# Optimization experiments

Measured on AMD Instinct MI355X. Metric: run time of the kernel, lower is better.

## Reference

```python
import jax, jax.numpy as jnp
import numpy as np

H = 768   # hidden_size
E = 9     # num_entity_types
R = 10    # num_relation_types
B, S, N = 8, 4096, 64
P = N * (N - 1) // 2  # 2016 ordered pairs i<j


def setup_inputs() -> dict:
    key = jax.random.key(0)
    ks = jax.random.split(key, 10)
    sd = 0.02
    return {
        "sequence_output": jax.random.normal(ks[0], (B, S, H), jnp.float32),
        "attention_mask": jnp.ones((B, S), jnp.int32),
        "entity_spans": jnp.sort(jax.random.randint(ks[1], (B, N, 2), 0, S), axis=-1),
        # entity_classifier: Linear(H, H//2) -> ReLU -> Linear(H//2, E)
        "w1": jax.random.normal(ks[2], (H, H // 2), jnp.float32) * sd,
        "b1": jnp.zeros((H // 2,), jnp.float32),
        "w2": jax.random.normal(ks[3], (H // 2, E), jnp.float32) * sd,
        "b2": jnp.zeros((E,), jnp.float32),
        # relation_classifier: Linear(2H, H) -> ReLU -> Linear(H, R)
        "rw1": jax.random.normal(ks[4], (2 * H, H), jnp.float32) * sd,
        "rb1": jnp.zeros((H,), jnp.float32),
        "rw2": jax.random.normal(ks[5], (H, R), jnp.float32) * sd,
        "rb2": jnp.zeros((R,), jnp.float32),
    }


def reference(sequence_output, attention_mask, entity_spans,
              w1, b1, w2, b2, rw1, rb1, rw2, rb2):
    # entity classifier over all tokens (dropout is identity in eval)
    h = jax.nn.relu(jnp.einsum('bsh,hf->bsf', sequence_output, w1) + b1)
    entity_logits = jnp.einsum('bsf,fe->bse', h, w2) + b2  # [B,S,E]

    # span mean-pooling via a [B,N,S] membership mask (segment-mean)
    pos = jnp.arange(S)
    start = entity_spans[..., 0:1]  # [B,N,1]
    end = entity_spans[..., 1:2]    # [B,N,1]
    mask = ((pos >= start) & (pos < end)).astype(sequence_output.dtype)  # [B,N,S]
    counts = jnp.clip(mask.sum(-1, keepdims=True), 1.0)  # avoid /0 for empty spans
    entity_reprs = jnp.einsum('bns,bsh->bnh', mask, sequence_output) / counts  # [B,N,H]
    pooled_logits = jnp.einsum('bns,bse->bne', mask, entity_logits) / counts   # [B,N,E]
    entity_types = jnp.argmax(pooled_logits, axis=-1)  # [B,N]

    # all i<j pairs, batched relation classifier (replaces per-pair Python loop)
    ii, jj = np.triu_indices(N, k=1)  # static index sets, len P
    pair = jnp.concatenate([entity_reprs[:, ii], entity_reprs[:, jj]], axis=-1)  # [B,P,2H]
    rh = jax.nn.relu(jnp.einsum('bpk,kh->bph', pair, rw1) + rb1)
    relation_logits = jnp.einsum('bph,hr->bpr', rh, rw2) + rb2  # [B,P,R]
    relation_types = jnp.argmax(relation_logits, axis=-1)  # [B,P]

    return entity_logits, relation_logits, entity_reprs, entity_types, relation_types
```

## Files before the change

kernel.cpp:

```cpp
#include <hip/hip_runtime.h>
#include <hip/hip_bf16.h>

#define Hh 768
#define Ff 384
#define Ee 9
#define Rr 10
#define Bb 8
#define Ss 4096
#define Nn_ENT 64
#define Pp 2016
#define CH 16
#define NC 256

typedef short bf16x8 __attribute__((ext_vector_type(8)));
typedef float f32x4 __attribute__((ext_vector_type(4)));

__device__ __forceinline__ void async_copy16(void* lds, const void* g) {
  auto* l = (__attribute__((address_space(3))) unsigned int*)(lds);
  auto* p = (const __attribute__((address_space(1))) unsigned int*)(g);
  __builtin_amdgcn_global_load_lds(p, l, 16, 0, 0);
}

__global__ __launch_bounds__(256) void transpose_w1(const float* __restrict__ w1,
                                                    unsigned short* __restrict__ wt) {
  __shared__ unsigned short tile[64][65];
  const int bk = blockIdx.x * 64;
  const int bc = blockIdx.y * 64;
  const int c = threadIdx.x & 63, kq = threadIdx.x >> 6;
#pragma unroll
  for (int i = 0; i < 16; ++i) {
    int k = kq * 16 + i;
    float v = w1[(size_t)(bk + k) * Ff + bc + c];
    tile[c][k] = __bfloat16_as_ushort(__float2bfloat16(v));
  }
  __syncthreads();
  const int k2 = threadIdx.x & 63, cq = threadIdx.x >> 6;
#pragma unroll
  for (int i = 0; i < 16; ++i) {
    int c2 = cq * 16 + i;
    wt[(size_t)(bc + c2) * Hh + bk + k2] = tile[c2][k2];
  }
}

__global__ __launch_bounds__(192) void seq_prep(const float* __restrict__ seq,
                                                unsigned short* __restrict__ seq16,
                                                float* __restrict__ Pc) {
  const int c = blockIdx.x, b = blockIdx.y;
  const int t = threadIdx.x;
  const size_t base = ((size_t)b * Ss + (size_t)c * CH) * Hh;
  const float4* p = (const float4*)(seq + base) + t;
  ushort4* q = (ushort4*)(seq16 + base) + t;
  float4 acc = {0.f, 0.f, 0.f, 0.f};
#pragma unroll
  for (int s = 0; s < CH; ++s) {
    float4 v = p[(size_t)s * (Hh / 4)];
    acc.x += v.x; acc.y += v.y; acc.z += v.z; acc.w += v.w;
    ushort4 o;
    o.x = __bfloat16_as_ushort(__float2bfloat16(v.x));
    o.y = __bfloat16_as_ushort(__float2bfloat16(v.y));
    o.z = __bfloat16_as_ushort(__float2bfloat16(v.z));
    o.w = __bfloat16_as_ushort(__float2bfloat16(v.w));
    q[(size_t)s * (Hh / 4)] = o;
  }
  ((float4*)(Pc + ((size_t)b * NC + c) * Hh))[t] = acc;
}

__global__ __launch_bounds__(512, 4) void gemm1_fused(const unsigned short* __restrict__ A,
                                                      const unsigned short* __restrict__ Wt,
                                                      const float* __restrict__ b1,
                                                      const float* __restrict__ w2,
                                                      const float* __restrict__ b2,
                                                      float* __restrict__ elog) {
  __shared__ unsigned short AB[(64 + 384) * 64];
  __shared__ float w2s[Ff * Ee];
  __shared__ float b1s[Ff];
  __shared__ float b2s[Ee];
  unsigned short* As = AB;
  unsigned short* Bs = AB + 64 * 64;
  float* red = (float*)AB;

  const int t = threadIdx.x;
  const int wid = t >> 6, lane = t & 63;
  const int wm = wid >> 2, wn = wid & 3;
  const int fr = lane & 15, fq = lane >> 4;
  const int row0 = blockIdx.x * 64;

  for (int i = t; i < Ff * Ee; i += 512) w2s[i] = w2[i];
  for (int i = t; i < Ff; i += 512) b1s[i] = b1[i];
  if (t < Ee) b2s[t] = b2[t];

  const int sg = (t & 7) ^ ((t >> 3) & 7);
  const unsigned short* aA = A + (size_t)(row0 + (t >> 3)) * Hh + sg * 8;
  const unsigned short* aB = Wt + (size_t)(t >> 3) * Hh + sg * 8;

  f32x4 acc[2][6] = {};

  for (int ks = 0; ks < Hh / 64; ++ks) {
    const int k0 = ks * 64;
    async_copy16(&As[wid * 512], aA + k0);
#pragma unroll
    for (int i = 0; i < 6; ++i)
      async_copy16(&Bs[i * 4096 + wid * 512], aB + (size_t)i * 64 * Hh + k0);
    __syncthreads();
#pragma unroll
    for (int kk = 0; kk < 2; ++kk) {
      const int g2 = ((kk * 4 + fq) ^ (fr & 7)) * 8;
      bf16x8 af[2], bfr[6];
#pragma unroll
      for (int m = 0; m < 2; ++m)
        af[m] = *(const bf16x8*)&As[(wm * 32 + m * 16 + fr) * 64 + g2];
#pragma unroll
      for (int n = 0; n < 6; ++n)
        bfr[n] = *(const bf16x8*)&Bs[(wn * 96 + n * 16 + fr) * 64 + g2];
#pragma unroll
      for (int m = 0; m < 2; ++m)
#pragma unroll
        for (int n = 0; n < 6; ++n)
          acc[m][n] = __builtin_amdgcn_mfma_f32_16x16x32_bf16(af[m], bfr[n], acc[m][n], 0, 0, 0);
    }
    __syncthreads();
  }

#pragma unroll
  for (int m = 0; m < 2; ++m) {
#pragma unroll
    for (int j = 0; j < 4; ++j) {
      float p[Ee];
#pragma unroll
      for (int e = 0; e < Ee; ++e) p[e] = 0.f;
#pragma unroll
      for (int n = 0; n < 6; ++n) {
        const int col = wn * 96 + n * 16 + fr;
        const float hv = fmaxf(acc[m][n][j] + b1s[col], 0.f);
        const float* wrow = &w2s[col * Ee];
#pragma unroll
        for (int e = 0; e < Ee; ++e) p[e] = fmaf(hv, wrow[e], p[e]);
      }
#pragma unroll
      for (int mask = 1; mask <= 8; mask <<= 1)
#pragma unroll
        for (int e = 0; e < Ee; ++e) p[e] += __shfl_xor(p[e], mask);
      if (fr < Ee) {
        const int row = wm * 32 + m * 16 + fq * 4 + j;
        red[(wn * 64 + row) * Ee + fr] = p[fr];
      }
    }
  }
  __syncthreads();
  for (int idx = t; idx < 64 * Ee; idx += 512) {
    const int row = idx / Ee, e = idx - row * Ee;
    float v = red[(0 * 64 + row) * Ee + e] + red[(1 * 64 + row) * Ee + e]
            + red[(2 * 64 + row) * Ee + e] + red[(3 * 64 + row) * Ee + e] + b2s[e];
    elog[(size_t)(row0 + row) * Ee + e] = v;
  }
}

__global__ __launch_bounds__(256) void gemm_uv_splitk(const float* __restrict__ A,
                                                      const float* __restrict__ rw1,
                                                      float* __restrict__ part) {
  const int uv = blockIdx.z & 1, ks = blockIdx.z >> 1;
  const float* Wp = rw1 + (size_t)uv * Hh * Hh + (size_t)ks * 192 * Hh;
  __shared__ float Ast[16][68];
  __shared__ float Wst[16][68];
  const int t = threadIdx.x;
  const int row0 = blockIdx.x * 64, col0 = blockIdx.y * 64;
  const int tm = (t & 15) * 4, tn = (t >> 4) * 4;
  const int lr = t >> 2, lk = (t & 3) * 4;
  const int wk = t >> 4, wc = (t & 15) * 4;
  float acc[4][4] = {};
  const float* Arow = A + (size_t)(row0 + lr) * Hh + ks * 192 + lk;
  for (int k0 = 0; k0 < 192; k0 += 16) {
    float4 av = *(const float4*)(Arow + k0);
    Ast[lk + 0][lr] = av.x; Ast[lk + 1][lr] = av.y;
    Ast[lk + 2][lr] = av.z; Ast[lk + 3][lr] = av.w;
    *(float4*)&Wst[wk][wc] = *(const float4*)(Wp + (size_t)(k0 + wk) * Hh + col0 + wc);
    __syncthreads();
#pragma unroll
    for (int kk = 0; kk < 16; ++kk) {
      const float4 a = *(const float4*)&Ast[kk][tm];
      const float4 b = *(const float4*)&Wst[kk][tn];
      acc[0][0] = fmaf(a.x, b.x, acc[0][0]); acc[0][1] = fmaf(a.x, b.y, acc[0][1]);
      acc[0][2] = fmaf(a.x, b.z, acc[0][2]); acc[0][3] = fmaf(a.x, b.w, acc[0][3]);
      acc[1][0] = fmaf(a.y, b.x, acc[1][0]); acc[1][1] = fmaf(a.y, b.y, acc[1][1]);
      acc[1][2] = fmaf(a.y, b.z, acc[1][2]); acc[1][3] = fmaf(a.y, b.w, acc[1][3]);
      acc[2][0] = fmaf(a.z, b.x, acc[2][0]); acc[2][1] = fmaf(a.z, b.y, acc[2][1]);
      acc[2][2] = fmaf(a.z, b.z, acc[2][2]); acc[2][3] = fmaf(a.z, b.w, acc[2][3]);
      acc[3][0] = fmaf(a.w, b.x, acc[3][0]); acc[3][1] = fmaf(a.w, b.y, acc[3][1]);
      acc[3][2] = fmaf(a.w, b.z, acc[3][2]); acc[3][3] = fmaf(a.w, b.w, acc[3][3]);
    }
    __syncthreads();
  }
  float* out = part + ((size_t)ks * 2 + uv) * (512 * Hh);
#pragma unroll
  for (int i = 0; i < 4; ++i) {
    float4 o; o.x = acc[i][0]; o.y = acc[i][1]; o.z = acc[i][2]; o.w = acc[i][3];
    *(float4*)(out + (size_t)(row0 + tm + i) * Hh + col0 + tn) = o;
  }
}

__global__ __launch_bounds__(256) void uv_reduce(const float* __restrict__ part,
                                                 float* __restrict__ uv) {
  const int i = blockIdx.x * 256 + threadIdx.x;
  const float4* p = (const float4*)part;
  float4 a = p[i], b = p[i + 196608], c = p[i + 2 * 196608], d = p[i + 3 * 196608];
  float4 o;
  o.x = (a.x + b.x) + (c.x + d.x);
  o.y = (a.y + b.y) + (c.y + d.y);
  o.z = (a.z + b.z) + (c.z + d.z);
  o.w = (a.w + b.w) + (c.w + d.w);
  ((float4*)uv)[i] = o;
}

__global__ __launch_bounds__(256) void chunk_scan(float* __restrict__ Pc) {
  __shared__ float tile[NC][64];
  const int b = blockIdx.y;
  const int h0 = blockIdx.x * 64;
  float* base = Pc + (size_t)b * NC * Hh + h0;
  const int l = threadIdx.x & 63, g = threadIdx.x >> 6;
#pragma unroll 4
  for (int c = g * 64; c < g * 64 + 64; ++c)
    tile[c][l] = base[(size_t)c * Hh + l];
  __syncthreads();
  float run = 0.f;
#pragma unroll 4
  for (int c = g * 64; c < g * 64 + 64; ++c) {
    run += tile[c][l];
    tile[c][l] = run;
  }
  __syncthreads();
  float off = 0.f;
#pragma unroll
  for (int gg = 0; gg < 3; ++gg)
    if (gg < g) off += tile[gg * 64 + 63][l];
  __syncthreads();
  if (g > 0) {
#pragma unroll 4
    for (int c = g * 64; c < g * 64 + 64; ++c)
      tile[c][l] += off;
  }
  __syncthreads();
#pragma unroll 4
  for (int c = g * 64; c < g * 64 + 64; ++c)
    base[(size_t)c * Hh + l] = tile[c][l];
}

__global__ __launch_bounds__(192) void entity_reprs_k(const float* __restrict__ seq,
                                                      const float* __restrict__ Pc,
                                                      const int* __restrict__ spans,
                                                      float* __restrict__ reprs) {
  const int bn = blockIdx.x;
  const int b = bn >> 6;
  const int start = spans[bn * 2], end = spans[bn * 2 + 1];
  const int cnt = max(end - start, 1);
  const float inv = 1.0f / (float)cnt;
  const int cs = (start + CH - 1) >> 4, ce = end >> 4;
  const float* seqb = seq + (size_t)b * Ss * Hh;
  const float4* Pcb = (const float4*)(Pc + (size_t)b * NC * Hh);
  const int t = threadIdx.x;
  float4 acc = {0.f, 0.f, 0.f, 0.f};
  if (cs <= ce) {
    if (cs < ce) {
      float4 hi = Pcb[(size_t)(ce - 1) * 192 + t];
      acc.x += hi.x; acc.y += hi.y; acc.z += hi.z; acc.w += hi.w;
      if (cs > 0) {
        float4 lo = Pcb[(size_t)(cs - 1) * 192 + t];
        acc.x -= lo.x; acc.y -= lo.y; acc.z -= lo.z; acc.w -= lo.w;
      }
    }
    for (int s = start; s < cs * CH; ++s) {
      float4 v = ((const float4*)(seqb + (size_t)s * Hh))[t];
      acc.x += v.x; acc.y += v.y; acc.z += v.z; acc.w += v.w;
    }
    for (int s = ce * CH; s < end; ++s) {
      float4 v = ((const float4*)(seqb + (size_t)s * Hh))[t];
      acc.x += v.x; acc.y += v.y; acc.z += v.z; acc.w += v.w;
    }
  } else {
    for (int s = start; s < end; ++s) {
      float4 v = ((const float4*)(seqb + (size_t)s * Hh))[t];
      acc.x += v.x; acc.y += v.y; acc.z += v.z; acc.w += v.w;
    }
  }
  float4 o; o.x = acc.x * inv; o.y = acc.y * inv; o.z = acc.z * inv; o.w = acc.w * inv;
  ((float4*)(reprs + (size_t)bn * Hh))[t] = o;
}

__global__ __launch_bounds__(256) void pooled_argmax(const float* __restrict__ elog,
                                                     const int* __restrict__ spans,
                                                     float* __restrict__ etypes) {
  __shared__ float red[4][Ee];
  const int bn = blockIdx.x;
  const int b = bn >> 6;
  const int start = spans[bn * 2], end = spans[bn * 2 + 1];
  const int t = threadIdx.x, lane = t & 63, w = t >> 6;
  float acc[Ee];
#pragma unroll
  for (int e = 0; e < Ee; ++e) acc[e] = 0.f;
  const float* p = elog + (size_t)b * Ss * Ee;
  for (int s = start + t; s < end; s += 256) {
    const float* q = p + (size_t)s * Ee;
#pragma unroll
    for (int e = 0; e < Ee; ++e) acc[e] += q[e];
  }
#pragma unroll
  for (int off = 32; off; off >>= 1)
#pragma unroll
    for (int e = 0; e < Ee; ++e) acc[e] += __shfl_down(acc[e], off);
  if (lane == 0) {
#pragma unroll
    for (int e = 0; e < Ee; ++e) red[w][e] = acc[e];
  }
  __syncthreads();
  if (t == 0) {
    int best = 0; float bv = -1e30f;
#pragma unroll
    for (int e = 0; e < Ee; ++e) {
      float v = red[0][e] + red[1][e] + red[2][e] + red[3][e];
      if (v > bv) { bv = v; best = e; }
    }
    etypes[bn] = (float)best;
  }
}

__global__ __launch_bounds__(256) void relations_k(const float* __restrict__ UV,
                                                   const float* __restrict__ rb1,
                                                   const float* __restrict__ rw2,
                                                   const float* __restrict__ rb2,
                                                   float* __restrict__ rlogits,
                                                   float* __restrict__ rtypes) {
  __shared__ float w2l[Hh * 11];
  __shared__ float b1l[Hh];
  const int t = threadIdx.x;
  for (int i = t; i < Hh * Rr; i += 256) {
    const int k = i / Rr, r = i - k * Rr;
    w2l[k * 11 + r] = rw2[i];
  }
  for (int i = t; i < Hh; i += 256) b1l[i] = rb1[i];
  __syncthreads();

  const int p = blockIdx.x * 4 + (t >> 6);
  const int lane = t & 63;
  const int b = p / Pp, pp = p % Pp;
  int i = 0, off = 0;
  while (off + (Nn_ENT - 1 - i) <= pp) { off += Nn_ENT - 1 - i; ++i; }
  const int j = i + 1 + (pp - off);
  const float* u = UV + ((size_t)b * Nn_ENT + i) * Hh;
  const float* v = UV + (size_t)512 * Hh + ((size_t)b * Nn_ENT + j) * Hh;
  float acc[Rr];
#pragma unroll
  for (int r = 0; r < Rr; ++r) acc[r] = 0.f;
  for (int k = lane; k < Hh; k += 64) {
    float x = fmaxf(u[k] + v[k] + b1l[k], 0.f);
    const float* w = &w2l[k * 11];
#pragma unroll
    for (int r = 0; r < Rr; ++r) acc[r] = fmaf(x, w[r], acc[r]);
  }
#pragma unroll
  for (int off2 = 32; off2; off2 >>= 1)
#pragma unroll
    for (int r = 0; r < Rr; ++r) acc[r] += __shfl_down(acc[r], off2);
  if (lane == 0) {
    int best = 0; float bv = acc[0] + rb2[0];
    rlogits[(size_t)p * Rr + 0] = bv;
#pragma unroll
    for (int r = 1; r < Rr; ++r) {
      float val = acc[r] + rb2[r];
      rlogits[(size_t)p * Rr + r] = val;
      if (val > bv) { bv = val; best = r; }
    }
    rtypes[p] = (float)best;
  }
}

extern "C" void kernel_launch(void* const* d_in, const int* in_sizes, int n_in,
                              void* d_out, int out_size, void* d_ws, size_t ws_size,
                              hipStream_t stream) {
  const float* seq   = (const float*)d_in[0];
  const int*   spans = (const int*)d_in[2];
  const float* w1    = (const float*)d_in[3];
  const float* b1    = (const float*)d_in[4];
  const float* w2    = (const float*)d_in[5];
  const float* b2    = (const float*)d_in[6];
  const float* rw1   = (const float*)d_in[7];
  const float* rb1   = (const float*)d_in[8];
  const float* rw2   = (const float*)d_in[9];
  const float* rb2   = (const float*)d_in[10];

  float* out_elog = (float*)d_out;
  float* out_rlog = out_elog + 294912;
  float* out_repr = out_rlog + 161280;
  float* out_etyp = out_repr + 393216;
  float* out_rtyp = out_etyp + 512;

  unsigned short* ws_s16 = (unsigned short*)d_ws;
  float*          ws_pc  = (float*)((char*)d_ws + 50331648);
  float*          ws_uv  = (float*)((char*)d_ws + 56623104);
  unsigned short* ws_wt  = (unsigned short*)((char*)d_ws + 59768832);
  float*          ws_uvp = (float*)((char*)d_ws + 60358656);

  transpose_w1<<<dim3(12, 6), 256, 0, stream>>>(w1, ws_wt);
  seq_prep<<<dim3(NC, Bb), 192, 0, stream>>>(seq, ws_s16, ws_pc);
  gemm1_fused<<<512, 512, 0, stream>>>(ws_s16, ws_wt, b1, w2, b2, out_elog);
  chunk_scan<<<dim3(Hh / 64, Bb), 256, 0, stream>>>(ws_pc);
  entity_reprs_k<<<512, 192, 0, stream>>>(seq, ws_pc, spans, out_repr);
  gemm_uv_splitk<<<dim3(8, 12, 8), 256, 0, stream>>>(out_repr, rw1, ws_uvp);
  uv_reduce<<<768, 256, 0, stream>>>(ws_uvp, ws_uv);
  pooled_argmax<<<512, 256, 0, stream>>>(out_elog, spans, out_etyp);
  relations_k<<<4032, 256, 0, stream>>>(ws_uv, rb1, rw2, rb2, out_rlog, out_rtyp);
}
```

Before: 162.6 us.

## Double-buffer gemm1 LDS tiles with K-step 32 to overlap loads and MFMA

Changes the fused entity GEMM main loop from a single 64-wide K tile per iteration to two alternating 32-wide K buffers. The next tile's async global-to-LDS copies are issued before computing on the current tile, so one barrier per step replaces two and load latency can overlap the MFMAs. The swizzle and per-wave copy mapping are reworked for the narrower tile. This doubles the iteration count and keeps only one compute step between barriers, so the overlap it gains may be small.

```diff
diff --git a/kernel.cpp b/kernel.cpp
--- a/kernel.cpp
+++ b/kernel.cpp
@@ -71,13 +71,11 @@
                                                       const float* __restrict__ w2,
                                                       const float* __restrict__ b2,
                                                       float* __restrict__ elog) {
-  __shared__ unsigned short AB[(64 + 384) * 64];
+  __shared__ unsigned short AB[2][448 * 32];
   __shared__ float w2s[Ff * Ee];
   __shared__ float b1s[Ff];
   __shared__ float b2s[Ee];
-  unsigned short* As = AB;
-  unsigned short* Bs = AB + 64 * 64;
-  float* red = (float*)AB;
+  float* red = (float*)&AB[0][0];
 
   const int t = threadIdx.x;
   const int wid = t >> 6, lane = t & 63;
@@ -89,37 +87,52 @@
   for (int i = t; i < Ff; i += 512) b1s[i] = b1[i];
   if (t < Ee) b2s[t] = b2[t];
 
-  const int sg = (t & 7) ^ ((t >> 3) & 7);
-  const unsigned short* aA = A + (size_t)(row0 + (t >> 3)) * Hh + sg * 8;
-  const unsigned short* aB = Wt + (size_t)(t >> 3) * Hh + sg * 8;
+  const int lrow = lane >> 2;
+  const int sgr = (lane & 3) ^ (lrow & 3);
+  const unsigned short* aApt = A + (size_t)(row0 + wid * 16 + lrow) * Hh + sgr * 8;
+  const unsigned short* aB0 = Wt + (size_t)((wid * 3 + 0) * 16 + lrow) * Hh + sgr * 8;
+  const unsigned short* aB1 = Wt + (size_t)((wid * 3 + 1) * 16 + lrow) * Hh + sgr * 8;
+  const unsigned short* aB2 = Wt + (size_t)((wid * 3 + 2) * 16 + lrow) * Hh + sgr * 8;
+
+#define STAGE(buf, ks) do {                                                  \
+    const int k0s = (ks) * 32;                                               \
+    if (wid < 4) async_copy16(&AB[buf][wid * 512], aApt + k0s);              \
+    async_copy16(&AB[buf][2048 + (wid * 3 + 0) * 512], aB0 + k0s);           \
+    async_copy16(&AB[buf][2048 + (wid * 3 + 1) * 512], aB1 + k0s);           \
+    async_copy16(&AB[buf][2048 + (wid * 3 + 2) * 512], aB2 + k0s);           \
+  } while (0)
 
   f32x4 acc[2][6] = {};
 
-  for (int ks = 0; ks < Hh / 64; ++ks) {
-    const int k0 = ks * 64;
-    async_copy16(&As[wid * 512], aA + k0);
-#pragma unroll
-    for (int i = 0; i < 6; ++i)
-      async_copy16(&Bs[i * 4096 + wid * 512], aB + (size_t)i * 64 * Hh + k0);
-    __syncthreads();
-#pragma unroll
-    for (int kk = 0; kk < 2; ++kk) {
-      const int g2 = ((kk * 4 + fq) ^ (fr & 7)) * 8;
-      bf16x8 af[2], bfr[6];
-#pragma unroll
-      for (int m = 0; m < 2; ++m)
-        af[m] = *(const bf16x8*)&As[(wm * 32 + m * 16 + fr) * 64 + g2];
+  STAGE(0, 0);
+  __syncthreads();
+
+  int cur = 0;
+  for (int ks = 0; ks < Hh / 32; ++ks) {
+    const bool more = ks < (Hh / 32) - 1;
+    if (more) STAGE(cur ^ 1, ks + 1);
+    const unsigned short* AsC = &AB[cur][0];
+    const unsigned short* BsC = &AB[cur][2048];
+    const int g2 = (fq ^ (fr & 3)) * 8;
+    bf16x8 af[2], bfr[6];
+#pragma unroll
+    for (int m = 0; m < 2; ++m)
+      af[m] = *(const bf16x8*)&AsC[(wm * 32 + m * 16 + fr) * 32 + g2];
+#pragma unroll
+    for (int n = 0; n < 6; ++n)
+      bfr[n] = *(const bf16x8*)&BsC[(wn * 96 + n * 16 + fr) * 32 + g2];
+#pragma unroll
+    for (int m = 0; m < 2; ++m)
 #pragma unroll
       for (int n = 0; n < 6; ++n)
-        bfr[n] = *(const bf16x8*)&Bs[(wn * 96 + n * 16 + fr) * 64 + g2];
-#pragma unroll
-      for (int m = 0; m < 2; ++m)
-#pragma unroll
-        for (int n = 0; n < 6; ++n)
-          acc[m][n] = __builtin_amdgcn_mfma_f32_16x16x32_bf16(af[m], bfr[n], acc[m][n], 0, 0, 0);
-    }
-    __syncthreads();
-  }
+        acc[m][n] = __builtin_amdgcn_mfma_f32_16x16x32_bf16(af[m], bfr[n], acc[m][n], 0, 0, 0);
+    if (more) {
+      __syncthreads();
+      cur ^= 1;
+    }
+  }
+#undef STAGE
+  __syncthreads();
 
 #pragma unroll
   for (int m = 0; m < 2; ++m) {
```

New measurement: 174.1 us. +7.1%, slower.

## Fuse bf16 conversion and chunk prefix sums into entity GEMM

Applied to the files above, without the earlier changes.

Removes the seq_prep kernel that converted the fp32 sequence to bf16 and computed per-16-row chunk sums. The GEMM now async-loads fp32 tiles of the sequence into swizzled LDS, converts them to bf16 in registers before the MFMAs, and computes the chunk sums from the same LDS tile with shuffle reductions. This avoids writing and re-reading a 50MB bf16 copy, at the cost of double the A-tile LDS footprint, more LDS read traffic and extra conversion work inside the GEMM loop.

```diff
diff --git a/kernel.cpp b/kernel.cpp
--- a/kernel.cpp
+++ b/kernel.cpp
@@ -42,81 +42,108 @@
   }
 }
 
-__global__ __launch_bounds__(192) void seq_prep(const float* __restrict__ seq,
-                                                unsigned short* __restrict__ seq16,
-                                                float* __restrict__ Pc) {
-  const int c = blockIdx.x, b = blockIdx.y;
-  const int t = threadIdx.x;
-  const size_t base = ((size_t)b * Ss + (size_t)c * CH) * Hh;
-  const float4* p = (const float4*)(seq + base) + t;
-  ushort4* q = (ushort4*)(seq16 + base) + t;
-  float4 acc = {0.f, 0.f, 0.f, 0.f};
-#pragma unroll
-  for (int s = 0; s < CH; ++s) {
-    float4 v = p[(size_t)s * (Hh / 4)];
-    acc.x += v.x; acc.y += v.y; acc.z += v.z; acc.w += v.w;
-    ushort4 o;
-    o.x = __bfloat16_as_ushort(__float2bfloat16(v.x));
-    o.y = __bfloat16_as_ushort(__float2bfloat16(v.y));
-    o.z = __bfloat16_as_ushort(__float2bfloat16(v.z));
-    o.w = __bfloat16_as_ushort(__float2bfloat16(v.w));
-    q[(size_t)s * (Hh / 4)] = o;
-  }
-  ((float4*)(Pc + ((size_t)b * NC + c) * Hh))[t] = acc;
-}
-
-__global__ __launch_bounds__(512, 4) void gemm1_fused(const unsigned short* __restrict__ A,
+__global__ __launch_bounds__(512, 4) void gemm1_fused(const float* __restrict__ A,
                                                       const unsigned short* __restrict__ Wt,
                                                       const float* __restrict__ b1,
                                                       const float* __restrict__ w2,
                                                       const float* __restrict__ b2,
-                                                      float* __restrict__ elog) {
-  __shared__ unsigned short AB[(64 + 384) * 64];
+                                                      float* __restrict__ elog,
+                                                      float* __restrict__ Pc) {
+  __shared__ float As[64 * 64];
+  __shared__ unsigned short Bs[384 * 64];
   __shared__ float w2s[Ff * Ee];
   __shared__ float b1s[Ff];
   __shared__ float b2s[Ee];
-  unsigned short* As = AB;
-  unsigned short* Bs = AB + 64 * 64;
-  float* red = (float*)AB;
+  float* red = (float*)&Bs[0];
 
   const int t = threadIdx.x;
   const int wid = t >> 6, lane = t & 63;
   const int wm = wid >> 2, wn = wid & 3;
   const int fr = lane & 15, fq = lane >> 4;
   const int row0 = blockIdx.x * 64;
+  const int bb = row0 >> 12;
+  const int c0 = (row0 & (Ss - 1)) >> 4;
 
   for (int i = t; i < Ff * Ee; i += 512) w2s[i] = w2[i];
   for (int i = t; i < Ff; i += 512) b1s[i] = b1[i];
   if (t < Ee) b2s[t] = b2[t];
 
-  const int sg = (t & 7) ^ ((t >> 3) & 7);
-  const unsigned short* aA = A + (size_t)(row0 + (t >> 3)) * Hh + sg * 8;
-  const unsigned short* aB = Wt + (size_t)(t >> 3) * Hh + sg * 8;
+  const int arow0 = (lane >> 4);
+  const int agr = lane & 15;
+  const int brow0 = (lane >> 3);
+  const int bgr = lane & 7;
 
   f32x4 acc[2][6] = {};
-
+  const int sB = ((fr & 7)) ;
+  const int swA = ((fr & 7) << 1);
+
+#pragma unroll 1
   for (int ks = 0; ks < Hh / 64; ++ks) {
     const int k0 = ks * 64;
-    async_copy16(&As[wid * 512], aA + k0);
-#pragma unroll
-    for (int i = 0; i < 6; ++i)
-      async_copy16(&Bs[i * 4096 + wid * 512], aB + (size_t)i * 64 * Hh + k0);
+#pragma unroll
+    for (int i = 0; i < 2; ++i) {
+      const int rl = (wid * 2 + i) * 4 + arow0;
+      const int g = agr ^ ((rl & 7) << 1);
+      async_copy16(&As[(wid * 2 + i) * 256],
+                   A + (size_t)(row0 + rl) * Hh + k0 + g * 4);
+    }
+#pragma unroll
+    for (int j = 0; j < 6; ++j) {
+      const int e = wid * 6 + j;
+      const int rl = e * 8 + brow0;
+      const int g = bgr ^ (rl & 7);
+      async_copy16(&Bs[e * 512],
+                   Wt + (size_t)rl * Hh + k0 + g * 8);
+    }
     __syncthreads();
+
 #pragma unroll
     for (int kk = 0; kk < 2; ++kk) {
-      const int g2 = ((kk * 4 + fq) ^ (fr & 7)) * 8;
       bf16x8 af[2], bfr[6];
 #pragma unroll
-      for (int m = 0; m < 2; ++m)
-        af[m] = *(const bf16x8*)&As[(wm * 32 + m * 16 + fr) * 64 + g2];
+      for (int m = 0; m < 2; ++m) {
+        const int R = wm * 32 + m * 16 + fr;
+        const int s0 = (2 * (kk * 4 + fq)) ^ swA;
+        const float* ap = &As[R * 64 + s0 * 4];
+        float4 v0 = ((const float4*)ap)[0];
+        float4 v1 = ((const float4*)ap)[1];
+        union { bf16x8 v; __hip_bfloat162 h2[4]; } u;
+        u.h2[0] = __float22bfloat162_rn(float2{v0.x, v0.y});
+        u.h2[1] = __float22bfloat162_rn(float2{v0.z, v0.w});
+        u.h2[2] = __float22bfloat162_rn(float2{v1.x, v1.y});
+        u.h2[3] = __float22bfloat162_rn(float2{v1.z, v1.w});
+        af[m] = u.v;
+      }
+      const int gB = ((kk * 4 + fq) ^ sB) * 8;
 #pragma unroll
       for (int n = 0; n < 6; ++n)
-        bfr[n] = *(const bf16x8*)&Bs[(wn * 96 + n * 16 + fr) * 64 + g2];
+        bfr[n] = *(const bf16x8*)&Bs[(wn * 96 + n * 16 + fr) * 64 + gB];
 #pragma unroll
       for (int m = 0; m < 2; ++m)
 #pragma unroll
         for (int n = 0; n < 6; ++n)
           acc[m][n] = __builtin_amdgcn_mfma_f32_16x16x32_bf16(af[m], bfr[n], acc[m][n], 0, 0, 0);
+    }
+
+    {
+      const int cc = t >> 7, kq = (t >> 3) & 15, rg = t & 7;
+      float4 s = {0.f, 0.f, 0.f, 0.f};
+#pragma unroll
+      for (int q = 0; q < 2; ++q) {
+        const int row = cc * 16 + rg * 2 + q;
+        const int slot = kq ^ ((row & 7) << 1);
+        float4 v = *(const float4*)&As[row * 64 + slot * 4];
+        s.x += v.x; s.y += v.y; s.z += v.z; s.w += v.w;
+      }
+#pragma unroll
+      for (int msk = 1; msk <= 4; msk <<= 1) {
+        s.x += __shfl_xor(s.x, msk);
+        s.y += __shfl_xor(s.y, msk);
+        s.z += __shfl_xor(s.z, msk);
+        s.w += __shfl_xor(s.w, msk);
+      }
+      if (rg == 0)
+        *(float4*)&Pc[((size_t)(bb * NC + c0 + cc)) * Hh + k0 + kq * 4] = s;
     }
     __syncthreads();
   }
@@ -392,15 +419,13 @@
   float* out_etyp = out_repr + 393216;
   float* out_rtyp = out_etyp + 512;
 
-  unsigned short* ws_s16 = (unsigned short*)d_ws;
-  float*          ws_pc  = (float*)((char*)d_ws + 50331648);
-  float*          ws_uv  = (float*)((char*)d_ws + 56623104);
-  unsigned short* ws_wt  = (unsigned short*)((char*)d_ws + 59768832);
-  float*          ws_uvp = (float*)((char*)d_ws + 60358656);
+  float*          ws_pc  = (float*)d_ws;
+  float*          ws_uv  = (float*)((char*)d_ws + 6291456);
+  unsigned short* ws_wt  = (unsigned short*)((char*)d_ws + 9437184);
+  float*          ws_uvp = (float*)((char*)d_ws + 10027008);
 
   transpose_w1<<<dim3(12, 6), 256, 0, stream>>>(w1, ws_wt);
-  seq_prep<<<dim3(NC, Bb), 192, 0, stream>>>(seq, ws_s16, ws_pc);
-  gemm1_fused<<<512, 512, 0, stream>>>(ws_s16, ws_wt, b1, w2, b2, out_elog);
+  gemm1_fused<<<512, 512, 0, stream>>>(seq, ws_wt, b1, w2, b2, out_elog, ws_pc);
   chunk_scan<<<dim3(Hh / 64, Bb), 256, 0, stream>>>(ws_pc);
   entity_reprs_k<<<512, 192, 0, stream>>>(seq, ws_pc, spans, out_repr);
   gemm_uv_splitk<<<dim3(8, 12, 8), 256, 0, stream>>>(out_repr, rw1, ws_uvp);
```

After: 174.7 us. 7.5% more time.
